# Kernel optimization log

Measured on AMD Instinct MI355X. Metric: run time of the kernel, lower is better.

The kernel has to match this reference:

```python
import jax, jax.numpy as jnp
import numpy as np

NUM_CLASSES = 20
NUM_ANCHORS = 3
BBOX_ATTRS = 5 + NUM_CLASSES
IMG_H = IMG_W = 416
IN_H = IN_W = 52
CONF_THRES = 0.5
NMS_THRES = 0.4
TOP_K = 2048


def setup_inputs() -> dict:
    key = jax.random.key(0)
    k1, _ = jax.random.split(key)
    inp = jax.random.normal(k1, (16, NUM_ANCHORS * BBOX_ATTRS, IN_H, IN_W), dtype=jnp.float32)
    anchors = jnp.array([[116.0, 90.0], [156.0, 198.0], [373.0, 326.0]], dtype=jnp.float32)
    return {"input": inp, "anchors": anchors}


def decode(inp, anchors):
    """YOLOv3 head decode (YOLOv3Loss.forward with targets=None).
    inp: [B, A*(5+C), H, W] -> output: [B, A*H*W, 5+C] with (cx, cy, w, h, conf, cls...)."""
    bs = inp.shape[0]
    stride_h = IMG_H / IN_H
    stride_w = IMG_W / IN_W
    scaled_anchors = anchors / jnp.array([stride_w, stride_h], dtype=inp.dtype)  # [A, 2]
    # [B, A, H, W, 5+C]
    pred = inp.reshape(bs, NUM_ANCHORS, BBOX_ATTRS, IN_H, IN_W).transpose(0, 1, 3, 4, 2)
    x = jax.nn.sigmoid(pred[..., 0])
    y = jax.nn.sigmoid(pred[..., 1])
    w = pred[..., 2]
    h = pred[..., 3]
    conf = jax.nn.sigmoid(pred[..., 4])
    pred_cls = jax.nn.sigmoid(pred[..., 5:])
    grid_x = jnp.arange(IN_W, dtype=inp.dtype)[None, None, None, :]
    grid_y = jnp.arange(IN_H, dtype=inp.dtype)[None, None, :, None]
    anchor_w = scaled_anchors[:, 0][None, :, None, None]
    anchor_h = scaled_anchors[:, 1][None, :, None, None]
    bx = (x + grid_x) * stride_w
    by = (y + grid_y) * stride_h
    bw = jnp.exp(w) * anchor_w * stride_w
    bh = jnp.exp(h) * anchor_h * stride_h
    boxes = jnp.stack([bx, by, bw, bh], axis=-1).reshape(bs, -1, 4)
    output = jnp.concatenate(
        [boxes, conf.reshape(bs, -1, 1), pred_cls.reshape(bs, -1, NUM_CLASSES)], axis=-1
    )
    return output


def _nms_one(corners, conf, cls_pred):
    """Greedy class-aware NMS over TOP_K conf-sorted candidates.
    corners: [K,4] x1y1x2y2, conf: [K] desc-sorted, cls_pred: [K] int32.
    Returns keep mask [K] bool."""
    x1, y1, x2, y2 = corners[:, 0], corners[:, 1], corners[:, 2], corners[:, 3]
    area = (x2 - x1 + 1.0) * (y2 - y1 + 1.0)
    ix1 = jnp.maximum(x1[:, None], x1[None, :])
    iy1 = jnp.maximum(y1[:, None], y1[None, :])
    ix2 = jnp.minimum(x2[:, None], x2[None, :])
    iy2 = jnp.minimum(y2[:, None], y2[None, :])
    inter = jnp.clip(ix2 - ix1 + 1.0, 0.0) * jnp.clip(iy2 - iy1 + 1.0, 0.0)
    iou = inter / (area[:, None] + area[None, :] - inter + 1e-16)
    # suppress j if kept i (earlier, higher conf, same class) overlaps >= thres
    cond = (iou >= NMS_THRES) & (cls_pred[:, None] == cls_pred[None, :])
    valid = conf >= CONF_THRES
    K = conf.shape[0]
    idx = jnp.arange(K)

    def body(i, carry):
        keep, supp = carry
        ki = valid[i] & (~supp[i])
        keep = keep.at[i].set(ki)
        supp = supp | (cond[i] & (idx > i) & ki)
        return keep, supp

    keep, _ = jax.lax.fori_loop(0, K, body, (jnp.zeros(K, bool), jnp.zeros(K, bool)))
    return keep


def reference(input, anchors):
    output = decode(input, anchors)  # [B, N, 5+C]
    conf = output[..., 4]
    # top-K candidates by objectness (desc order == conf sort in original NMS)
    top_conf, top_idx = jax.lax.top_k(conf, TOP_K)  # [B, K]
    boxes = output[..., :4]
    cx, cy, w, h = boxes[..., 0], boxes[..., 1], boxes[..., 2], boxes[..., 3]
    corners = jnp.stack([cx - w / 2, cy - h / 2, cx + w / 2, cy + h / 2], axis=-1)
    corners_s = jnp.take_along_axis(corners, top_idx[..., None], axis=1)  # [B, K, 4]
    cls_pred = jnp.argmax(output[..., 5:], axis=-1).astype(jnp.int32)  # [B, N]
    cls_s = jnp.take_along_axis(cls_pred, top_idx, axis=1)  # [B, K]
    keep = jax.vmap(_nms_one)(corners_s, top_conf, cls_s)  # [B, K] bool
    return output, top_idx, keep
```

## Files before the change

kernel.cpp:

```cpp
#include <hip/hip_runtime.h>

#pragma clang fp contract(off)

#define B 16
#define A 3
#define HGT 52
#define WID 52
#define HW 2704
#define NCAND 8112
#define CATTR 25
#define TOPK 2048
#define NWORD 64
#define CH 256
#define NCHUNK (TOPK / CH)
#define GPC (CH / 32)
#define CHP 260
#define EPT 8

typedef unsigned int uint32;
typedef unsigned long long u64;

__global__ __launch_bounds__(256) void decode_kernel(const float* __restrict__ inp,
                                                     const float* __restrict__ anchors,
                                                     float* __restrict__ out,
                                                     float* __restrict__ cws,
                                                     float* __restrict__ pk) {
    __shared__ float sm[256 * CATTR];
    int tid = threadIdx.x;
    int t = blockIdx.x * 256 + tid;
    int b  = t / NCAND;
    int n  = t - b * NCAND;
    int a  = n / HW;
    int hw = n - a * HW;
    int gy = hw / WID;
    int gx = hw - gy * WID;
    const float* ip = inp + ((size_t)(b * (A * CATTR) + a * CATTR)) * HW + hw;
    float* sp = sm + tid * CATTR;

    float p0 = ip[0 * HW], p1 = ip[1 * HW], p2 = ip[2 * HW], p3 = ip[3 * HW], p4 = ip[4 * HW];
    float sx = 1.0f / (1.0f + expf(-p0));
    float sy = 1.0f / (1.0f + expf(-p1));
    float bx = (sx + (float)gx) * 8.0f;
    float by = (sy + (float)gy) * 8.0f;
    float bw = expf(p2) * anchors[a * 2 + 0];
    float bh = expf(p3) * anchors[a * 2 + 1];
    float cf = 1.0f / (1.0f + expf(-p4));
    sp[0] = bx; sp[1] = by; sp[2] = bw; sp[3] = bh; sp[4] = cf;
    cws[t] = cf;

    float best = -1.0f; int bc = 0;
#pragma unroll
    for (int c = 0; c < 20; ++c) {
        float v = ip[(5 + c) * HW];
        float s = 1.0f / (1.0f + expf(-v));
        sp[5 + c] = s;
        if (s > best) { best = s; bc = c; }
    }

    float hw_ = bw * 0.5f, hh_ = bh * 0.5f;
    float x1 = bx - hw_, y1 = by - hh_, x2 = bx + hw_, y2 = by + hh_;
    float area = ((x2 - x1) + 1.0f) * ((y2 - y1) + 1.0f);
    float4* pk4 = (float4*)(pk + (size_t)t * 8);
    pk4[0] = make_float4(x1, y1, x2, y2);
    pk4[1] = make_float4(area, (float)bc, (cf >= 0.5f) ? 1.0f : 0.0f, 0.0f);

    __syncthreads();
    const float4* sm4 = (const float4*)sm;
    float4* o4 = (float4*)(out + (size_t)blockIdx.x * 256 * CATTR);
#pragma unroll
    for (int k = 0; k < 6; ++k) o4[k * 256 + tid] = sm4[k * 256 + tid];
    if (tid < 64) o4[1536 + tid] = sm4[1536 + tid];
}

__device__ __forceinline__ void cexd(u64& a, u64& b, bool up) {
    if ((a > b) == up) { u64 tmp = a; a = b; b = tmp; }
}

__device__ __forceinline__ u64 sel(u64 k, u64 o, bool kmin) {
    return kmin ? (k < o ? k : o) : (k > o ? k : o);
}

__global__ __launch_bounds__(256) void sort1_kernel(const float* __restrict__ conf,
                                                    u64* __restrict__ runs) {
    __shared__ u64 mb[2048];
    int blk = blockIdx.x;
    int b = blk >> 2, c = blk & 3;
    int t = threadIdx.x;
    int base = t * EPT;
    int gbase = c * 2048 + base;
    const float* cp = conf + b * NCAND;

    u64 key[EPT];
    if (gbase + EPT <= NCAND) {
        const float4* cp4 = (const float4*)(cp + gbase);
        float4 c0 = cp4[0], c1 = cp4[1];
        float cf[EPT] = {c0.x, c0.y, c0.z, c0.w, c1.x, c1.y, c1.z, c1.w};
#pragma unroll
        for (int e = 0; e < EPT; ++e) {
            unsigned bits = __float_as_uint(cf[e]) | 0x80000000u;
            key[e] = ((u64)(~bits) << 32) | (unsigned)(gbase + e);
        }
    } else {
#pragma unroll
        for (int e = 0; e < EPT; ++e) {
            int idx = gbase + e;
            if (idx < NCAND) {
                unsigned bits = __float_as_uint(cp[idx]) | 0x80000000u;
                key[e] = ((u64)(~bits) << 32) | (unsigned)idx;
            } else key[e] = ~0ull;
        }
    }

    cexd(key[0], key[1], true); cexd(key[2], key[3], false);
    cexd(key[4], key[5], true); cexd(key[6], key[7], false);

    cexd(key[0], key[2], true);  cexd(key[1], key[3], true);
    cexd(key[4], key[6], false); cexd(key[5], key[7], false);
    cexd(key[0], key[1], true);  cexd(key[2], key[3], true);
    cexd(key[4], key[5], false); cexd(key[6], key[7], false);

    bool up8 = ((t & 1) == 0);
    cexd(key[0], key[4], up8); cexd(key[1], key[5], up8);
    cexd(key[2], key[6], up8); cexd(key[3], key[7], up8);
    cexd(key[0], key[2], up8); cexd(key[1], key[3], up8);
    cexd(key[4], key[6], up8); cexd(key[5], key[7], up8);
    cexd(key[0], key[1], up8); cexd(key[2], key[3], up8);
    cexd(key[4], key[5], up8); cexd(key[6], key[7], up8);

    for (unsigned k = 16; k <= 2048; k <<= 1) {
        bool up = (((unsigned)base & k) == 0);
        for (unsigned j = k >> 1; j >= 8; j >>= 1) {
            unsigned m = j >> 3;
            bool kmin = (up == ((t & m) == 0));
            if (m >= 64) {
                __syncthreads();
#pragma unroll
                for (int e = 0; e < EPT; ++e) mb[e * 256 + t] = key[e];
                __syncthreads();
                int pt = t ^ (int)m;
#pragma unroll
                for (int e = 0; e < EPT; ++e) key[e] = sel(key[e], mb[e * 256 + pt], kmin);
            } else {
#pragma unroll
                for (int e = 0; e < EPT; ++e) {
                    u64 o = __shfl_xor(key[e], (int)m);
                    key[e] = sel(key[e], o, kmin);
                }
            }
        }
        cexd(key[0], key[4], up); cexd(key[1], key[5], up);
        cexd(key[2], key[6], up); cexd(key[3], key[7], up);
        cexd(key[0], key[2], up); cexd(key[1], key[3], up);
        cexd(key[4], key[6], up); cexd(key[5], key[7], up);
        cexd(key[0], key[1], up); cexd(key[2], key[3], up);
        cexd(key[4], key[5], up); cexd(key[6], key[7], up);
    }

    u64* R = runs + ((size_t)b * 4 + c) * 2048;
#pragma unroll
    for (int e = 0; e < EPT; ++e) R[base + e] = key[e];
}

__device__ __forceinline__ u64 merge_rank(const u64* __restrict__ Aa,
                                          const u64* __restrict__ Bb, int r) {
    int lo = 0, hi = r;
    while (lo < hi) {
        int mid = (lo + hi) >> 1;
        if (Aa[mid] < Bb[r - 1 - mid]) lo = mid + 1; else hi = mid;
    }
    u64 av = Aa[lo], bv = Bb[r - lo];
    return av < bv ? av : bv;
}

__global__ __launch_bounds__(256) void merge1_kernel(const u64* __restrict__ runs,
                                                     u64* __restrict__ mruns) {
    int t  = blockIdx.x * 256 + threadIdx.x;
    int bp = t >> 11;
    int r  = t & 2047;
    const u64* Aa = runs + (size_t)bp * 4096;
    const u64* Bb = Aa + 2048;
    mruns[(size_t)bp * 2048 + r] = merge_rank(Aa, Bb, r);
}

__global__ __launch_bounds__(256) void merge2_kernel(const u64* __restrict__ mruns,
                                                     float* __restrict__ topf) {
    int t = blockIdx.x * 256 + threadIdx.x;
    int b = t >> 11;
    int r = t & 2047;
    const u64* Aa = mruns + (size_t)b * 4096;
    const u64* Bb = Aa + 2048;
    u64 key = merge_rank(Aa, Bb, r);
    topf[t] = (float)(unsigned)(key & 0xFFFFFFFFu);
}

__global__ __launch_bounds__(256) void geo_kernel(const float* __restrict__ pk,
                                                  const float* __restrict__ topf,
                                                  float* __restrict__ gx1,
                                                  float* __restrict__ gy1,
                                                  float* __restrict__ gx2,
                                                  float* __restrict__ gy2,
                                                  float* __restrict__ gar,
                                                  uint32* __restrict__ gcv,
                                                  uint32* __restrict__ vwords) {
    int t = blockIdx.x * 256 + threadIdx.x;
    int b = t >> 11;
    int idx = (int)topf[t];
    const float4* p4 = (const float4*)(pk + ((size_t)b * NCAND + idx) * 8);
    float4 g0 = p4[0], g1 = p4[1];
    gx1[t] = g0.x; gy1[t] = g0.y; gx2[t] = g0.z; gy2[t] = g0.w;
    gar[t] = g1.x;
    gcv[t] = (uint32)g1.y;
    bool valid = (g1.z != 0.0f);
    unsigned long long bal = __ballot(valid);
    if ((t & 63) == 0) {
        vwords[(t >> 5) + 0] = (uint32)bal;
        vwords[(t >> 5) + 1] = (uint32)(bal >> 32);
    }
}

#define KMID (13421772.5 / 33554432.0)
__global__ __launch_bounds__(1024) void build_kernel(const float* __restrict__ gx1,
                                                     const float* __restrict__ gy1,
                                                     const float* __restrict__ gx2,
                                                     const float* __restrict__ gy2,
                                                     const float* __restrict__ gar,
                                                     const uint32* __restrict__ gcv,
                                                     uint32* __restrict__ rowmask) {
    __shared__ float  x1s[TOPK], y1s[TOPK], x2s[TOPK], y2s[TOPK];
    __shared__ uint32 clss[TOPK];
    int bt   = blockIdx.y;
    int pr   = blockIdx.x;
    int tid  = threadIdx.x;
    int lane = tid & 63;
    int wv   = tid >> 6;
    int base = bt * TOPK;
    uint32* rmT = rowmask + (size_t)base * NWORD;

    for (int j = tid; j < TOPK; j += 1024) {
        int g = base + j;
        x1s[j] = gx1[g]; y1s[j] = gy1[g]; x2s[j] = gx2[g]; y2s[j] = gy2[g];
        clss[j] = gcv[g] & 0xffu;
    }
    __syncthreads();

    int r  = (wv >> 3) ? (31 - pr) : pr;
    int i0 = r * 64 + (wv & 7) * 8;

    float rx1[8], ry1[8], rx2[8], ry2[8], rar[8];
    uint32 rcl[8];
#pragma unroll
    for (int k = 0; k < 8; ++k) {
        rx1[k] = x1s[i0 + k]; ry1[k] = y1s[i0 + k];
        rx2[k] = x2s[i0 + k]; ry2[k] = y2s[i0 + k];
        rar[k] = ((rx2[k] - rx1[k]) + 1.0f) * ((ry2[k] - ry1[k]) + 1.0f);
        rcl[k] = clss[i0 + k];
    }

    int j0 = r * 64 + lane;
    float cx1 = x1s[j0], cy1 = y1s[j0], cx2 = x2s[j0], cy2 = y2s[j0];
    uint32 cc = clss[j0];

    for (int cg = r; cg < 32; ++cg) {
        float nx1 = 0.f, ny1 = 0.f, nx2 = 0.f, ny2 = 0.f; uint32 nc = 0;
        if (cg + 1 < 32) {
            int nj = (cg + 1) * 64 + lane;
            nx1 = x1s[nj]; ny1 = y1s[nj]; nx2 = x2s[nj]; ny2 = y2s[nj];
            nc = clss[nj];
        }
        float car = ((cx2 - cx1) + 1.0f) * ((cy2 - cy1) + 1.0f);
        u64 bal[8];
#pragma unroll
        for (int k = 0; k < 8; ++k) {
            float ix1 = fmaxf(rx1[k], cx1);
            float iy1 = fmaxf(ry1[k], cy1);
            float ix2 = fminf(rx2[k], cx2);
            float iy2 = fminf(ry2[k], cy2);
            float iw = fmaxf((ix2 - ix1) + 1.0f, 0.0f);
            float ih = fmaxf((iy2 - iy1) + 1.0f, 0.0f);
            float inter = iw * ih;
            float denom = ((rar[k] + car) - inter) + 1e-16f;
            bool cond = ((double)inter > KMID * (double)denom) && (cc == rcl[k]);
            bal[k] = __ballot(cond);
        }
        u64 v = bal[0];
#pragma unroll
        for (int k = 1; k < 8; ++k) if ((lane & 7) == k) v = bal[k];
        uint32 w32 = (lane & 8) ? (uint32)(v >> 32) : (uint32)v;
        int gi = i0 + (lane & 7);
        int wd = 2 * cg + ((lane >> 3) & 1);
        if (wd == (gi >> 5)) w32 &= ~((2u << (gi & 31)) - 1u);
        if (lane < 16) rmT[(size_t)wd * TOPK + gi] = w32;
        cx1 = nx1; cy1 = ny1; cx2 = nx2; cy2 = ny2; cc = nc;
    }
}

__device__ __forceinline__ void copy_chunk_dma(const uint32* __restrict__ rmT,
                                               uint32* dstL, int c, int wvm1, int lane) {
    int wmin = 8 * c;
    for (int w = wmin + wvm1; w < 64; w += 15) {
        const uint32* gp = rmT + (size_t)w * TOPK + c * CH + lane * 4;
        uint32* lp = dstL + w * CHP;
        __builtin_amdgcn_global_load_lds((const __attribute__((address_space(1))) void*)gp,
                                         (__attribute__((address_space(3))) void*)lp,
                                         16, 0, 0);
    }
}

__global__ __launch_bounds__(1024) void scan_kernel(const uint32* __restrict__ rowmask,
                                                    const uint32* __restrict__ vwords,
                                                    float* __restrict__ keepf) {
    __shared__ uint32 buf[2][64 * CHP];
    int bt  = blockIdx.x;
    int tid = threadIdx.x;
    int wv  = tid >> 6;
    int l   = tid & 63;
    const uint32* rmT = rowmask + (size_t)bt * TOPK * NWORD;

    uint32 supp = 0, keepw = 0;
    if (wv == 0) supp = ~vwords[bt * 64 + l];

    if (wv > 0) copy_chunk_dma(rmT, buf[0], 0, wv - 1, l);
    __syncthreads();

    for (int c = 0; c < NCHUNK; ++c) {
        if (wv > 0) {
            if (c + 1 < NCHUNK) copy_chunk_dma(rmT, buf[(c + 1) & 1], c + 1, wv - 1, l);
        } else {
            const uint32* bp = buf[c & 1];
            uint4 sq[8];
            {
                int g0 = c * GPC;
                const uint4* sp = (const uint4*)(bp + g0 * CHP);
#pragma unroll
                for (int q = 0; q < 8; ++q) sq[q] = sp[q];
            }
            for (int gl = 0; gl < GPC; ++gl) {
                int g = c * GPC + gl;
                uint4 rwq[8];
                const uint4* rp = (const uint4*)(bp + l * CHP + gl * 32);
#pragma unroll
                for (int q = 0; q < 8; ++q) rwq[q] = rp[q];
                uint32 cur = __builtin_amdgcn_readlane(supp, g);
#pragma unroll
                for (int q = 0; q < 8; ++q) {
                    uint32 s0 = sq[q].x, s1 = sq[q].y, s2 = sq[q].z, s3 = sq[q].w;
                    int k = q * 4;
                    cur |= s0 & ((((cur >> (k + 0)) & 1u)) - 1u);
                    cur |= s1 & ((((cur >> (k + 1)) & 1u)) - 1u);
                    cur |= s2 & ((((cur >> (k + 2)) & 1u)) - 1u);
                    cur |= s3 & ((((cur >> (k + 3)) & 1u)) - 1u);
                }
                uint32 keep = ~cur;
                if (l == g) keepw = keep;
                if (gl + 1 < GPC) {
                    const uint4* sp = (const uint4*)(bp + (g + 1) * CHP + (gl + 1) * 32);
#pragma unroll
                    for (int q = 0; q < 8; ++q) sq[q] = sp[q];
                }
                uint32 upd = 0;
#pragma unroll
                for (int q = 0; q < 8; ++q) {
                    int k = q * 4;
                    upd |= rwq[q].x & (uint32)(((int)(keep << (31 - (k + 0)))) >> 31);
                    upd |= rwq[q].y & (uint32)(((int)(keep << (31 - (k + 1)))) >> 31);
                    upd |= rwq[q].z & (uint32)(((int)(keep << (31 - (k + 2)))) >> 31);
                    upd |= rwq[q].w & (uint32)(((int)(keep << (31 - (k + 3)))) >> 31);
                }
                supp |= upd;
            }
        }
        __syncthreads();
    }

    if (wv == 0) {
#pragma unroll
        for (int k = 0; k < 32; ++k)
            keepf[bt * TOPK + l * 32 + k] = (float)((keepw >> k) & 1u);
    }
}

extern "C" void kernel_launch(void* const* d_in, const int* in_sizes, int n_in,
                              void* d_out, int out_size, void* d_ws, size_t ws_size,
                              hipStream_t stream) {
    const float* inp     = (const float*)d_in[0];
    const float* anchors = (const float*)d_in[1];
    float* out   = (float*)d_out;
    float* topf  = out  + (size_t)B * NCAND * CATTR;
    float* keepf = topf + (size_t)B * TOPK;

    float*  cws = (float*)d_ws;
    float*  pk  = cws + B * NCAND;
    float*  gx1 = pk  + (size_t)B * NCAND * 8;
    float*  gy1 = gx1 + B * TOPK;
    float*  gx2 = gy1 + B * TOPK;
    float*  gy2 = gx2 + B * TOPK;
    float*  gar = gy2 + B * TOPK;
    uint32* gcv = (uint32*)(gar + B * TOPK);
    uint32* rowmask = gcv + B * TOPK;
    uint32* vwords  = rowmask + (size_t)B * TOPK * NWORD;
    u64* runs  = (u64*)rowmask;
    u64* mruns = runs + (size_t)B * 4 * 2048;

    decode_kernel<<<(B * NCAND) / 256, 256, 0, stream>>>(inp, anchors, out, cws, pk);
    sort1_kernel<<<B * 4, 256, 0, stream>>>(cws, runs);
    merge1_kernel<<<(B * 2 * TOPK) / 256, 256, 0, stream>>>(runs, mruns);
    merge2_kernel<<<(B * TOPK) / 256, 256, 0, stream>>>(mruns, topf);
    geo_kernel<<<(B * TOPK) / 256, 256, 0, stream>>>(pk, topf, gx1, gy1, gx2, gy2, gar, gcv, vwords);
    build_kernel<<<dim3(16, B), 1024, 0, stream>>>(gx1, gy1, gx2, gy2, gar, gcv, rowmask);
    scan_kernel<<<B, 1024, 0, stream>>>(rowmask, vwords, keepf);
}
```

Baseline: 170.0 us.

## Fuse two merge passes and geometry gather into one per-batch LDS kernel

Replaces the merge1, merge2 and geo kernels with a single kernel that runs one 1024-thread block per batch image. The block loads the four sorted runs into shared memory, does both merge-path rounds there and gathers box geometry directly. This removes two kernel launches and the global round trips for intermediate merged runs and topf. In exchange only 16 blocks run, which lowers parallelism, and the block uses 96KB of LDS.

```diff
diff --git a/kernel.cpp b/kernel.cpp
--- a/kernel.cpp
+++ b/kernel.cpp
@@ -172,49 +172,57 @@
     return av < bv ? av : bv;
 }
 
-__global__ __launch_bounds__(256) void merge1_kernel(const u64* __restrict__ runs,
-                                                     u64* __restrict__ mruns) {
-    int t  = blockIdx.x * 256 + threadIdx.x;
-    int bp = t >> 11;
-    int r  = t & 2047;
-    const u64* Aa = runs + (size_t)bp * 4096;
-    const u64* Bb = Aa + 2048;
-    mruns[(size_t)bp * 2048 + r] = merge_rank(Aa, Bb, r);
-}
-
-__global__ __launch_bounds__(256) void merge2_kernel(const u64* __restrict__ mruns,
-                                                     float* __restrict__ topf) {
-    int t = blockIdx.x * 256 + threadIdx.x;
-    int b = t >> 11;
-    int r = t & 2047;
-    const u64* Aa = mruns + (size_t)b * 4096;
-    const u64* Bb = Aa + 2048;
-    u64 key = merge_rank(Aa, Bb, r);
-    topf[t] = (float)(unsigned)(key & 0xFFFFFFFFu);
-}
-
-__global__ __launch_bounds__(256) void geo_kernel(const float* __restrict__ pk,
-                                                  const float* __restrict__ topf,
-                                                  float* __restrict__ gx1,
-                                                  float* __restrict__ gy1,
-                                                  float* __restrict__ gx2,
-                                                  float* __restrict__ gy2,
-                                                  float* __restrict__ gar,
-                                                  uint32* __restrict__ gcv,
-                                                  uint32* __restrict__ vwords) {
-    int t = blockIdx.x * 256 + threadIdx.x;
-    int b = t >> 11;
-    int idx = (int)topf[t];
-    const float4* p4 = (const float4*)(pk + ((size_t)b * NCAND + idx) * 8);
-    float4 g0 = p4[0], g1 = p4[1];
-    gx1[t] = g0.x; gy1[t] = g0.y; gx2[t] = g0.z; gy2[t] = g0.w;
-    gar[t] = g1.x;
-    gcv[t] = (uint32)g1.y;
-    bool valid = (g1.z != 0.0f);
-    unsigned long long bal = __ballot(valid);
-    if ((t & 63) == 0) {
-        vwords[(t >> 5) + 0] = (uint32)bal;
-        vwords[(t >> 5) + 1] = (uint32)(bal >> 32);
+__global__ __launch_bounds__(1024) void topsel_kernel(const u64* __restrict__ runs,
+                                                      const float* __restrict__ pk,
+                                                      float* __restrict__ topf,
+                                                      float* __restrict__ gx1,
+                                                      float* __restrict__ gy1,
+                                                      float* __restrict__ gx2,
+                                                      float* __restrict__ gy2,
+                                                      float* __restrict__ gar,
+                                                      uint32* __restrict__ gcv,
+                                                      uint32* __restrict__ vwords) {
+    __shared__ u64 lds[12288];
+    int bt  = blockIdx.x;
+    int tid = threadIdx.x;
+    const u64* R = runs + (size_t)bt * 8192;
+
+#pragma unroll
+    for (int k = 0; k < 8; ++k) lds[tid + k * 1024] = R[tid + k * 1024];
+    __syncthreads();
+
+    u64* m = lds + 8192;
+    u64 v[4];
+#pragma unroll
+    for (int k = 0; k < 4; ++k) {
+        int o = tid + k * 1024;
+        int p = o >> 11, r = o & 2047;
+        const u64* Aa = lds + p * 4096;
+        const u64* Bb = Aa + 2048;
+        v[k] = merge_rank(Aa, Bb, r);
+    }
+#pragma unroll
+    for (int k = 0; k < 4; ++k) m[tid + k * 1024] = v[k];
+    __syncthreads();
+
+#pragma unroll
+    for (int k = 0; k < 2; ++k) {
+        int r = tid + k * 1024;
+        u64 key = merge_rank(m, m + 2048, r);
+        unsigned idx = (unsigned)(key & 0xFFFFFFFFu);
+        int t = bt * TOPK + r;
+        topf[t] = (float)idx;
+        const float4* p4 = (const float4*)(pk + ((size_t)bt * NCAND + idx) * 8);
+        float4 g0 = p4[0], g1 = p4[1];
+        gx1[t] = g0.x; gy1[t] = g0.y; gx2[t] = g0.z; gy2[t] = g0.w;
+        gar[t] = g1.x;
+        gcv[t] = (uint32)g1.y;
+        bool valid = (g1.z != 0.0f);
+        unsigned long long bal = __ballot(valid);
+        if ((tid & 63) == 0) {
+            vwords[(t >> 5) + 0] = (uint32)bal;
+            vwords[(t >> 5) + 1] = (uint32)(bal >> 32);
+        }
     }
 }
 
@@ -398,14 +406,11 @@
     uint32* gcv = (uint32*)(gar + B * TOPK);
     uint32* rowmask = gcv + B * TOPK;
     uint32* vwords  = rowmask + (size_t)B * TOPK * NWORD;
-    u64* runs  = (u64*)rowmask;
-    u64* mruns = runs + (size_t)B * 4 * 2048;
+    u64* runs = (u64*)rowmask;
 
     decode_kernel<<<(B * NCAND) / 256, 256, 0, stream>>>(inp, anchors, out, cws, pk);
     sort1_kernel<<<B * 4, 256, 0, stream>>>(cws, runs);
-    merge1_kernel<<<(B * 2 * TOPK) / 256, 256, 0, stream>>>(runs, mruns);
-    merge2_kernel<<<(B * TOPK) / 256, 256, 0, stream>>>(mruns, topf);
-    geo_kernel<<<(B * TOPK) / 256, 256, 0, stream>>>(pk, topf, gx1, gy1, gx2, gy2, gar, gcv, vwords);
+    topsel_kernel<<<B, 1024, 0, stream>>>(runs, pk, topf, gx1, gy1, gx2, gy2, gar, gcv, vwords);
     build_kernel<<<dim3(16, B), 1024, 0, stream>>>(gx1, gy1, gx2, gy2, gar, gcv, rowmask);
     scan_kernel<<<B, 1024, 0, stream>>>(rowmask, vwords, keepf);
 }
```

Result: no change. 169.4 us (median of 2 runs) (-0.3%).
